# Optimization experiments

Hardware: AMD Instinct MI355X
Metric: run time of the kernel (lower is better)

Reference implementation:

```python
import jax, jax.numpy as jnp
import numpy as np

T = 2048        # q_len (current chunk)
P = 2048        # past KV cache length
HID = 4096      # hidden_size
H = 32          # num_attention_heads
D = HID // H    # head_dim = 128
THETA = 10000.0


def apply_rope(x, pos):
    # x: [H, T, D], pos: [T] int
    half = D // 2
    inv_freq = 1.0 / (THETA ** (jnp.arange(0, half, dtype=jnp.float32) / half))
    ang = pos.astype(jnp.float32)[:, None] * inv_freq[None, :]      # [T, D/2]
    cos = jnp.concatenate([jnp.cos(ang), jnp.cos(ang)], axis=-1)[None]  # [1, T, D]
    sin = jnp.concatenate([jnp.sin(ang), jnp.sin(ang)], axis=-1)[None]
    rot = jnp.concatenate([-x[..., half:], x[..., :half]], axis=-1)
    return x * cos + rot * sin


def setup_inputs() -> dict:
    key = jax.random.key(0)
    ks = jax.random.split(key, 8)
    s = 1.0 / np.sqrt(HID)
    inp = {
        "hidden_states": jax.random.normal(ks[0], (T, HID), dtype=jnp.float32),
        "attention_mask": jnp.triu(jnp.full((T, T), -jnp.inf, dtype=jnp.float32), k=1),
        "Wq": jax.random.normal(ks[1], (HID, HID), dtype=jnp.float32) * s,
        "Wk": jax.random.normal(ks[2], (HID, HID), dtype=jnp.float32) * s,
        "Wv": jax.random.normal(ks[3], (HID, HID), dtype=jnp.float32) * s,
        "Wo": jax.random.normal(ks[4], (HID, HID), dtype=jnp.float32) * s,
        "past_k": jax.random.normal(ks[5], (H, P, D), dtype=jnp.float32),
        "past_v": jax.random.normal(ks[6], (H, P, D), dtype=jnp.float32),
        "position_ids": P + jnp.arange(T, dtype=jnp.int32),
        "past_length": P,
    }
    return inp


def reference(hidden_states, attention_mask, Wq, Wk, Wv, Wo, past_k, past_v,
              position_ids, past_length):
    # QKV projections -> [H, T, D]
    proj = lambda W: (hidden_states @ W).reshape(T, H, D).transpose(1, 0, 2)
    q, k, v = proj(Wq), proj(Wk), proj(Wv)
    q = apply_rope(q, position_ids)
    k = apply_rope(k, position_ids)

    scale = 1.0 / jnp.sqrt(jnp.float32(D))
    # scores against past cache and current chunk (fp32 softmax, as in source)
    past_dots = (jnp.einsum('htd,hsd->hts', q, past_k) * scale).astype(jnp.float32)
    pmask = jnp.where(jnp.arange(P) < past_length, 0.0, -jnp.inf)  # [P]
    past_dots = past_dots + pmask
    cur = ((jnp.einsum('htd,hsd->hts', q, k) * scale) + attention_mask).astype(jnp.float32)

    # online-softmax merge via logsumexp combination
    past_lse = jax.scipy.special.logsumexp(past_dots, axis=-1, keepdims=True)
    cur_lse = jax.scipy.special.logsumexp(cur, axis=-1, keepdims=True)
    tot_lse = jnp.logaddexp(past_lse, cur_lse)
    pw = jnp.exp(past_dots - tot_lse).astype(q.dtype)
    cw = jnp.exp(cur - tot_lse).astype(q.dtype)

    out = jnp.einsum('hts,hsd->htd', pw, past_v) + jnp.einsum('hts,hsd->htd', cw, v)
    out = jnp.where(past_length == 0,
                    jnp.einsum('hts,hsd->htd', jax.nn.softmax(cur, axis=-1).astype(q.dtype), v),
                    out)
    out = out.transpose(1, 0, 2).reshape(T, HID)   # [T, hidden]
    return out @ Wo
```

## Files before the change

kernel.cpp:

```cpp
#include <hip/hip_runtime.h>
#include <cstdint>
#include <cstddef>

#define T_LEN 2048
#define PAST_MAX 2048
#define HID 4096
#define NHEAD 32
#define DHEAD 128

typedef __bf16 bf16_t;
typedef __bf16 bf16x4 __attribute__((ext_vector_type(4)));
typedef __bf16 bf16x8 __attribute__((ext_vector_type(8)));
typedef float  f32x4  __attribute__((ext_vector_type(4)));
typedef float  f32x16 __attribute__((ext_vector_type(16)));
typedef unsigned int u32x4 __attribute__((ext_vector_type(4)));

__device__ __forceinline__ void gload16(const void* g, void* l){
  __builtin_amdgcn_global_load_lds((const __attribute__((address_space(1))) void*)g,
                                   (__attribute__((address_space(3))) void*)l,
                                   16, 0, 0);
}

__device__ __forceinline__ unsigned pack_bf16(float a, float b){
  const unsigned ua = __builtin_bit_cast(unsigned short, (bf16_t)a);
  const unsigned ub = __builtin_bit_cast(unsigned short, (bf16_t)b);
  return ua | (ub << 16);
}

__global__ void cvt2_k(const float* __restrict__ a, bf16_t* __restrict__ ao,
                       const float* __restrict__ b, bf16_t* __restrict__ bo, int n4){
  int i = blockIdx.x * 256 + threadIdx.x;
  if (i < n4){
    const float4 v = ((const float4*)a)[i];
    bf16x4 o = { (bf16_t)v.x, (bf16_t)v.y, (bf16_t)v.z, (bf16_t)v.w };
    ((bf16x4*)ao)[i] = o;
  } else {
    i -= n4;
    const float4 v = ((const float4*)b)[i];
    bf16x4 o = { (bf16_t)v.x, (bf16_t)v.y, (bf16_t)v.z, (bf16_t)v.w };
    ((bf16x4*)bo)[i] = o;
  }
}

__global__ __launch_bounds__(256) void transpose2_k(const float* __restrict__ in,
                                                    bf16_t* __restrict__ out, int R, int C){
  __shared__ float tile[64][65];
  const int r0 = blockIdx.x << 6, c0 = blockIdx.y << 6;
  const size_t bo = (size_t)blockIdx.z * (size_t)R * (size_t)C;
  const int tx = threadIdx.x & 15, ty = threadIdx.x >> 4;
#pragma unroll
  for (int k = 0; k < 4; ++k){
    const float4 v = *(const float4*)(in + bo + (size_t)(r0 + ty + 16*k) * C + c0 + tx*4);
    float* tp = &tile[ty + 16*k][tx*4];
    tp[0] = v.x; tp[1] = v.y; tp[2] = v.z; tp[3] = v.w;
  }
  __syncthreads();
  const int rr0 = (threadIdx.x & 7) * 8;
  const int ccb = threadIdx.x >> 3;
#pragma unroll
  for (int k = 0; k < 2; ++k){
    const int cc = ccb + 32*k;
    bf16x8 o;
#pragma unroll
    for (int j = 0; j < 8; ++j) o[j] = (bf16_t)tile[rr0 + j][cc];
    *(bf16x8*)(out + bo + (size_t)(c0 + cc) * R + r0 + rr0) = o;
  }
}

__global__ __launch_bounds__(256) void transpose3_k(
    const float* __restrict__ s0, const float* __restrict__ s1, const float* __restrict__ s2,
    bf16_t* __restrict__ d0, bf16_t* __restrict__ d1, bf16_t* __restrict__ d2){
  __shared__ float tile[64][65];
  const float* in = (blockIdx.z == 0) ? s0 : (blockIdx.z == 1) ? s1 : s2;
  bf16_t* out = (blockIdx.z == 0) ? d0 : (blockIdx.z == 1) ? d1 : d2;
  const int r0 = blockIdx.x << 6, c0 = blockIdx.y << 6;
  const int tx = threadIdx.x & 15, ty = threadIdx.x >> 4;
#pragma unroll
  for (int k = 0; k < 4; ++k){
    const float4 v = *(const float4*)(in + (size_t)(r0 + ty + 16*k) * HID + c0 + tx*4);
    float* tp = &tile[ty + 16*k][tx*4];
    tp[0] = v.x; tp[1] = v.y; tp[2] = v.z; tp[3] = v.w;
  }
  __syncthreads();
  const int rr0 = (threadIdx.x & 7) * 8;
  const int ccb = threadIdx.x >> 3;
#pragma unroll
  for (int k = 0; k < 2; ++k){
    const int cc = ccb + 32*k;
    bf16x8 o;
#pragma unroll
    for (int j = 0; j < 8; ++j) o[j] = (bf16_t)tile[rr0 + j][cc];
    *(bf16x8*)(out + (size_t)(c0 + cc) * HID + r0 + rr0) = o;
  }
}

__global__ void ropek_k(bf16_t* __restrict__ K, const int* __restrict__ pos){
  const int idx = blockIdx.x * 256 + threadIdx.x;
  const int i = idx & 63;
  const int t = (idx >> 6) & (T_LEN - 1);
  const int h = idx >> 17;
  const size_t base = ((size_t)h * T_LEN + t) * DHEAD;
  const float p = (float)pos[t];
  const float inv = __expf(-(float)i * 0.14391156605212898f);
  const float ang = p * inv;
  float sn, cs;
  sincosf(ang, &sn, &cs);
  const float b0 = (float)K[base + i], b1 = (float)K[base + i + 64];
  K[base + i]      = (bf16_t)(b0 * cs - b1 * sn);
  K[base + i + 64] = (bf16_t)(b1 * cs + b0 * sn);
}

#define QUAD384(PR, BF) \
  __builtin_amdgcn_s_setprio(1); \
  _Pragma("unroll") \
  for (int kk = 0; kk < 2; ++kk){ \
    _Pragma("unroll") \
    for (int mf = 0; mf < 4; ++mf){ \
      _Pragma("unroll") \
      for (int ni = 0; ni < 2; ++ni) \
        acc[mf][(PR)*2 + ni] = __builtin_amdgcn_mfma_f32_16x16x32_bf16( \
            af[mf][kk], BF[ni][kk], acc[mf][(PR)*2 + ni], 0, 0, 0); \
    } \
  } \
  __builtin_amdgcn_s_setprio(0);

__global__ __launch_bounds__(512, 1) void gemmqkv384_k(
    const bf16_t* __restrict__ A,
    const bf16_t* __restrict__ Bc,
    bf16_t* __restrict__ OQ, bf16_t* __restrict__ OK2, bf16_t* __restrict__ OVT)
{
  const int bid = blockIdx.x;
  const int wg  = (bid & 7) * 64 + (bid >> 3);
  const int mt  = wg & 15;
  const int nt  = wg >> 4;
  const int m0  = mt << 7;
  const int n0g = nt * 384;

  const int tid = threadIdx.x;
  const int wv = tid >> 6, lane = tid & 63, lm = lane & 15, g = lane >> 4;
  const int wr = wv >> 2, wc = wv & 3;

  __shared__ __align__(16) char smem[131072];

  const f32x4 fzero = {0.f, 0.f, 0.f, 0.f};
  f32x4 acc[4][6];
#pragma unroll
  for (int i = 0; i < 4; ++i)
#pragma unroll
    for (int j = 0; j < 6; ++j) acc[i][j] = fzero;

  size_t aoff[2], boff[2];
#pragma unroll
  for (int i = 0; i < 2; ++i){
    const int c = i * 512 + tid;
    const int u = c >> 3;
    const int j = ((c & 7) ^ (u & 7)) << 3;
    aoff[i] = (size_t)(m0 + u) * HID + j;
    const int bcol = (u >> 5) * 96 + (u & 31);
    boff[i] = (size_t)(n0g + bcol) * HID + j;
  }
  const int ldst0 = (wv * 64) << 4;
  const int ldst1 = (512 + wv * 64) << 4;

  auto stgA = [&](char* buf, int kt){
    const bf16_t* src = A + (size_t)kt * 64;
    gload16(src + aoff[0], buf + ldst0);
    gload16(src + aoff[1], buf + ldst1);
  };
  auto stgB = [&](char* buf, int kt, int pr){
    const bf16_t* src = Bc + (size_t)kt * 64 + (size_t)pr * (32 * HID);
    char* dst = buf + 16384 + pr * 16384;
    gload16(src + boff[0], dst + ldst0);
    gload16(src + boff[1], dst + ldst1);
  };

  const int koff0 = ((0 + g) ^ (lm & 7)) << 4;
  const int koff1 = ((4 + g) ^ (lm & 7)) << 4;
  const int abase = ((wr << 6) + lm) << 7;
  const int bbase = ((wc << 5) + lm) << 7;

  stgA(smem, 0); stgB(smem, 0, 0); stgB(smem, 0, 1); stgB(smem, 0, 2);
  stgA(smem + 65536, 1); stgB(smem + 65536, 1, 0); stgB(smem + 65536, 1, 1);
  asm volatile("s_waitcnt vmcnt(6)" ::: "memory");
  __builtin_amdgcn_s_barrier();

  bf16x8 af[4][2], bf[2][2];

  for (int kt = 0; kt < 64; ++kt){
    char* buf  = smem + (kt & 1) * 65536;
    char* obuf = smem + ((kt + 1) & 1) * 65536;

#pragma unroll
    for (int mf = 0; mf < 4; ++mf){
      af[mf][0] = *(const bf16x8*)(buf + abase + mf * 2048 + koff0);
      af[mf][1] = *(const bf16x8*)(buf + abase + mf * 2048 + koff1);
    }
#pragma unroll
    for (int ni = 0; ni < 2; ++ni){
      bf[ni][0] = *(const bf16x8*)(buf + 16384 + bbase + ni * 2048 + koff0);
      bf[ni][1] = *(const bf16x8*)(buf + 16384 + bbase + ni * 2048 + koff1);
    }
    if (kt + 1 < 64) stgB(obuf, kt + 1, 2);
    __builtin_amdgcn_sched_barrier(0);
    __builtin_amdgcn_s_barrier();
    asm volatile("s_waitcnt lgkmcnt(0)" ::: "memory");
    __builtin_amdgcn_sched_barrier(0);
    QUAD384(0, bf)
    __builtin_amdgcn_s_barrier();

#pragma unroll
    for (int ni = 0; ni < 2; ++ni){
      bf[ni][0] = *(const bf16x8*)(buf + 32768 + bbase + ni * 2048 + koff0);
      bf[ni][1] = *(const bf16x8*)(buf + 32768 + bbase + ni * 2048 + koff1);
    }
    if (kt + 2 < 64) stgA(buf, kt + 2);
    __builtin_amdgcn_sched_barrier(0);
    __builtin_amdgcn_s_barrier();
    asm volatile("s_waitcnt lgkmcnt(0)" ::: "memory");
    __builtin_amdgcn_sched_barrier(0);
    QUAD384(1, bf)
    __builtin_amdgcn_s_barrier();

#pragma unroll
    for (int ni = 0; ni < 2; ++ni){
      bf[ni][0] = *(const bf16x8*)(buf + 49152 + bbase + ni * 2048 + koff0);
      bf[ni][1] = *(const bf16x8*)(buf + 49152 + bbase + ni * 2048 + koff1);
    }
    if (kt + 2 < 64){ stgB(buf, kt + 2, 0); stgB(buf, kt + 2, 1); }
    __builtin_amdgcn_sched_barrier(0);
    __builtin_amdgcn_s_barrier();
    asm volatile("s_waitcnt lgkmcnt(0)" ::: "memory");
    __builtin_amdgcn_sched_barrier(0);
    QUAD384(2, bf)
    if (kt <= 61) asm volatile("s_waitcnt vmcnt(6)" ::: "memory");
    else          asm volatile("s_waitcnt vmcnt(0)" ::: "memory");
    __builtin_amdgcn_sched_barrier(0);
    __builtin_amdgcn_s_barrier();
  }

#pragma unroll
  for (int pr = 0; pr < 3; ++pr)
#pragma unroll
    for (int ni = 0; ni < 2; ++ni){
      const int colg = n0g + wc * 96 + pr * 32 + ni * 16 + lm;
      const int z  = colg >> 12;
      const int wi = colg & 4095;
      const int hh = wi >> 7, dd = wi & 127;
      const int ai = pr * 2 + ni;
#pragma unroll
      for (int mf = 0; mf < 4; ++mf){
        const int trow0 = m0 + wr * 64 + mf * 16 + g * 4;
        if (z == 2){
          bf16x4 v4 = { (bf16_t)acc[mf][ai][0], (bf16_t)acc[mf][ai][1],
                        (bf16_t)acc[mf][ai][2], (bf16_t)acc[mf][ai][3] };
          *(bf16x4*)(OVT + ((size_t)hh * DHEAD + dd) * T_LEN + trow0) = v4;
        } else {
          bf16_t* ob = z ? OK2 : OQ;
#pragma unroll
          for (int r = 0; r < 4; ++r)
            ob[((size_t)hh * T_LEN + trow0 + r) * DHEAD + dd] = (bf16_t)acc[mf][ai][r];
        }
      }
    }
}

__global__ __launch_bounds__(512, 1) void gemm4p_k(
    const bf16_t* __restrict__ A, const bf16_t* __restrict__ B,
    float* __restrict__ OF, int cpx)
{
  const int bid = blockIdx.x;
  const int wg  = (bid & 7) * cpx + (bid >> 3);
  const int mt  = wg & 7;
  const int nt  = wg >> 3;
  const int m0  = mt << 8;
  const int n0  = nt << 7;

  const int tid = threadIdx.x;
  const int wv = tid >> 6, lane = tid & 63, lm = lane & 15, g = lane >> 4;
  const int wr = wv >> 1, wc = wv & 1;

  __shared__ __align__(16) char smem[98304];

  const f32x4 fzero = {0.f, 0.f, 0.f, 0.f};
  f32x4 acc[4][4];
#pragma unroll
  for (int i = 0; i < 4; ++i)
#pragma unroll
    for (int j = 0; j < 4; ++j) acc[i][j] = fzero;

  int srow[2], schk[2];
#pragma unroll
  for (int i = 0; i < 2; ++i){
    const int c = i * 512 + tid;
    srow[i] = c >> 3;
    schk[i] = (c & 7) ^ (srow[i] & 7);
  }
  const int sdst0 = ((0 * 512 + wv * 64) << 4);
  const int sdst1 = ((1 * 512 + wv * 64) << 4);

  auto stg = [&](int kt, int op){
    if (kt < 64){
      char* dst = smem + (kt & 1) * 49152 + op * 16384;
      const bf16_t* base = (op < 2) ? A + (size_t)(m0 + (op << 7)) * HID
                                    : B + (size_t)n0 * HID;
      base += kt * 64;
      gload16(base + (size_t)srow[0] * HID + schk[0] * 8, dst + sdst0);
      gload16(base + (size_t)srow[1] * HID + schk[1] * 8, dst + sdst1);
    }
  };

  const int koff0 = ((g)     ^ (lm & 7)) << 4;
  const int koff1 = ((4 + g) ^ (lm & 7)) << 4;
  const int abase = ((wr >> 1) << 14) + ((((wr & 1) << 6) + lm) << 7);
  const int bbase = 32768 + ((((wc << 6)) + lm) << 7);

  bf16x8 bfr[4][2];
  auto dsB = [&](int buf){
    const char* p = smem + buf * 49152 + bbase;
#pragma unroll
    for (int ni = 0; ni < 4; ++ni){
      bfr[ni][0] = *(const bf16x8*)(p + ni * 2048 + koff0);
      bfr[ni][1] = *(const bf16x8*)(p + ni * 2048 + koff1);
    }
  };

  stg(0, 2);
  stg(0, 0); stg(0, 1);
  stg(1, 2);
  asm volatile("s_waitcnt vmcnt(2)" ::: "memory");
  __builtin_amdgcn_s_barrier();

  for (int t = 0; t < 32; ++t){
    const int c0 = 2 * t, c1 = 2 * t + 1;
    const bool last = (t == 31);

#pragma unroll
    for (int half = 0; half < 2; ++half){
      const char* bufp = smem + half * 49152;
      bf16x8 afr[2][2];
      dsB(half);
#pragma unroll
      for (int mf = 0; mf < 2; ++mf){
        afr[mf][0] = *(const bf16x8*)(bufp + abase + mf * 2048 + koff0);
        afr[mf][1] = *(const bf16x8*)(bufp + abase + mf * 2048 + koff1);
      }
      if (half == 0){ stg(c1, 0); stg(c1, 1); }
      else          { stg(c0 + 2, 0); stg(c0 + 2, 1); }
      __builtin_amdgcn_s_barrier();
      asm volatile("s_waitcnt lgkmcnt(0)" ::: "memory");
      __builtin_amdgcn_s_setprio(1);
#pragma unroll
      for (int kk = 0; kk < 2; ++kk)
#pragma unroll
        for (int mf = 0; mf < 2; ++mf)
#pragma unroll
          for (int ni = 0; ni < 4; ++ni)
            acc[mf][ni] = __builtin_amdgcn_mfma_f32_16x16x32_bf16(afr[mf][kk], bfr[ni][kk], acc[mf][ni], 0, 0, 0);
      __builtin_amdgcn_s_setprio(0);
      __builtin_amdgcn_s_barrier();

#pragma unroll
      for (int mf = 0; mf < 2; ++mf){
        afr[mf][0] = *(const bf16x8*)(bufp + abase + (mf + 2) * 2048 + koff0);
        afr[mf][1] = *(const bf16x8*)(bufp + abase + (mf + 2) * 2048 + koff1);
      }
      if (half == 0) stg(c0 + 2, 2);
      else           stg(c1 + 2, 2);
      if (last) asm volatile("s_waitcnt vmcnt(0)" ::: "memory");
      else      asm volatile("s_waitcnt vmcnt(2)" ::: "memory");
      __builtin_amdgcn_s_barrier();
      asm volatile("s_waitcnt lgkmcnt(0)" ::: "memory");
      __builtin_amdgcn_s_setprio(1);
#pragma unroll
      for (int kk = 0; kk < 2; ++kk)
#pragma unroll
        for (int mf = 0; mf < 2; ++mf)
#pragma unroll
          for (int ni = 0; ni < 4; ++ni)
            acc[mf + 2][ni] = __builtin_amdgcn_mfma_f32_16x16x32_bf16(afr[mf][kk], bfr[ni][kk], acc[mf + 2][ni], 0, 0, 0);
      __builtin_amdgcn_s_setprio(0);
      __builtin_amdgcn_s_barrier();
    }
  }

#pragma unroll
  for (int ni = 0; ni < 4; ++ni){
    const int col = n0 + wc * 64 + ni * 16 + lm;
#pragma unroll
    for (int mf = 0; mf < 4; ++mf)
#pragma unroll
      for (int r = 0; r < 4; ++r){
        const int trow = m0 + wr * 64 + mf * 16 + g * 4 + r;
        OF[(size_t)trow * HID + col] = acc[mf][ni][r];
      }
  }
}

__global__ __launch_bounds__(256, 2) void attn2_k(
    const bf16_t* __restrict__ Q,
    const bf16_t* __restrict__ Kc,
    const bf16_t* __restrict__ VTc,
    const bf16_t* __restrict__ Kp,
    const bf16_t* __restrict__ VTp,
    bf16_t* __restrict__ Ctx,
    const int* __restrict__ plen_p,
    const int* __restrict__ pos)
{
  const int bid = blockIdx.x;
  const int xcd = bid & 7;
  const int k   = bid >> 3;
  const int ho  = k >> 4;
  const int qraw= k & 15;
  const int h   = (xcd << 2) | ho;
  const int qb  = (ho & 2) ? (15 - qraw) : qraw;

  const int tid = threadIdx.x;
  const int w = tid >> 6, lane = tid & 63, l31 = lane & 31, hi = lane >> 5;
  const int qw0 = qb * 128 + w * 32;
  const int qrow = qw0 + l31;
  const int plen = plen_p[0];
  const int npast = (plen + 63) >> 6;
  const int NT = npast + 2 * qb + 2;

  __shared__ __align__(16) char smem[65536 + 512];
  float* lred = (float*)(smem + 65536);

  const bf16_t* qbase = Q + ((size_t)h * T_LEN + qrow) * DHEAD;
  bf16x8 qf[8];
#pragma unroll
  for (int dc = 0; dc < 8; ++dc)
    qf[dc] = *(const bf16x8*)(qbase + dc * 16 + 8 * hi);
  {
    const float ppos = (float)pos[qrow];
    const float qs = 0.08838834764831845f;
#pragma unroll
    for (int dc = 0; dc < 4; ++dc)
#pragma unroll
      for (int j = 0; j < 8; ++j){
        const int fi = dc * 16 + 8 * hi + j;
        const float invf = __expf(-(float)fi * 0.14391156605212898f);
        float sn, cs;
        sincosf(ppos * invf, &sn, &cs);
        const float a0 = (float)qf[dc][j], a1 = (float)qf[dc + 4][j];
        qf[dc][j]     = (bf16_t)((a0 * cs - a1 * sn) * qs);
        qf[dc + 4][j] = (bf16_t)((a1 * cs + a0 * sn) * qs);
      }
  }
  __builtin_amdgcn_sched_barrier(0);

  const f32x16 fz = {0.f,0.f,0.f,0.f,0.f,0.f,0.f,0.f,0.f,0.f,0.f,0.f,0.f,0.f,0.f,0.f};
  f32x16 o[4] = {fz, fz, fz, fz};
  float m = -1e30f, l = 0.f;

  auto stage = [&](int t, int buf){
    const bf16_t* kb; const bf16_t* vb;
    if (t < npast){
      const int s0 = t * 64;
      kb = Kp  + ((size_t)h * PAST_MAX + s0) * DHEAD;
      vb = VTp + (size_t)h * DHEAD * PAST_MAX + s0;
    } else {
      const int s0 = (t - npast) * 64;
      kb = Kc  + ((size_t)h * T_LEN + s0) * DHEAD;
      vb = VTc + (size_t)h * DHEAD * T_LEN + s0;
    }
    char* kl = smem + buf * 32768;
    char* vl = kl + 16384;
#pragma unroll
    for (int i = 0; i < 4; ++i){
      const int c = i * 256 + w * 64 + lane;
      const int krow = c >> 4, kcol = c & 15;
      gload16(kb + (size_t)krow * DHEAD + ((kcol ^ (krow & 7)) << 3), kl + (i * 256 + w * 64) * 16);
      const int vrow = c >> 3, vcol = c & 7;
      gload16(vb + (size_t)vrow * 2048 + ((vcol ^ (vrow & 7)) << 3), vl + (i * 256 + w * 64) * 16);
    }
  };

  stage(0, 0);
  __builtin_amdgcn_sched_barrier(0);

  for (int t = 0; t < NT; ++t){
    const int cur = t & 1;
    if (t + 1 < NT){
      stage(t + 1, cur ^ 1);
      asm volatile("s_waitcnt vmcnt(8)" ::: "memory");
    } else {
      asm volatile("s_waitcnt vmcnt(0)" ::: "memory");
    }
    __builtin_amdgcn_sched_barrier(0);
    __builtin_amdgcn_s_barrier();
    __builtin_amdgcn_sched_barrier(0);

    const bool isc = (t >= npast);
    const int s0c = (t - npast) * 64;
    const bool active = !isc || (s0c <= qw0 + 31);

    if (active){
      char* kl = smem + cur * 32768;
      char* vl = kl + 16384;

      f32x16 sacc[2] = {fz, fz};
      __builtin_amdgcn_s_setprio(1);
#pragma unroll
      for (int kvh = 0; kvh < 2; ++kvh){
        const int krow = (kvh << 5) + l31;
        const int kbo = krow << 8;
        const int sw = (krow & 7) << 4;
#pragma unroll
        for (int dc = 0; dc < 8; ++dc){
          const bf16x8 kf = *(const bf16x8*)(kl + kbo + ((dc * 32 + 16 * hi) ^ sw));
          sacc[kvh] = __builtin_amdgcn_mfma_f32_32x32x16_bf16(kf, qf[dc], sacc[kvh], 0, 0, 0);
        }
      }
      __builtin_amdgcn_s_setprio(0);

      const bool mcur  = isc && (s0c + 63 > qw0);
      const bool mpast = !isc && ((t + 1) * 64 > plen);
      float pv[2][16];
      float pm = -1e30f;
      if (mcur | mpast){
#pragma unroll
        for (int kvh = 0; kvh < 2; ++kvh)
#pragma unroll
          for (int r = 0; r < 16; ++r){
            float x = sacc[kvh][r];
            const int kvoff = (kvh << 5) + (r & 3) + 8 * (r >> 2) + 4 * hi;
            if (mcur  && (s0c + kvoff >  qrow)) x = -1e30f;
            if (mpast && (t * 64 + kvoff >= plen)) x = -1e30f;
            pv[kvh][r] = x;
            pm = fmaxf(pm, x);
          }
      } else {
#pragma unroll
        for (int kvh = 0; kvh < 2; ++kvh)
#pragma unroll
          for (int r = 0; r < 16; ++r){
            pv[kvh][r] = sacc[kvh][r];
            pm = fmaxf(pm, sacc[kvh][r]);
          }
      }
      pm = fmaxf(pm, __shfl_xor(pm, 32));

      if (!__all(pm - m <= 8.f)){
        const float mn = fmaxf(m, pm);
        const float corr = __expf(m - mn);
        m = mn;
        l *= corr;
        if (hi == 0) lred[(w << 5) + l31] = corr;
        asm volatile("s_waitcnt lgkmcnt(0)" ::: "memory");
#pragma unroll
        for (int r = 0; r < 16; ++r){
          const float cc = lred[(w << 5) + (r & 3) + 8 * (r >> 2) + 4 * hi];
#pragma unroll
          for (int nb = 0; nb < 4; ++nb) o[nb][r] *= cc;
        }
      }

      float sum = 0.f;
#pragma unroll
      for (int kvh = 0; kvh < 2; ++kvh)
#pragma unroll
        for (int r = 0; r < 16; ++r){
          const float pe = __expf(pv[kvh][r] - m);
          pv[kvh][r] = pe;
          sum += pe;
        }
      sum += __shfl_xor(sum, 32);
      l += sum;

      unsigned wds[2][8];
#pragma unroll
      for (int kvh = 0; kvh < 2; ++kvh)
#pragma unroll
        for (int i = 0; i < 8; ++i)
          wds[kvh][i] = pack_bf16(pv[kvh][2 * i], pv[kvh][2 * i + 1]);

      bf16x8 pf[4];
#pragma unroll
      for (int ks = 0; ks < 4; ++ks){
        const int s = ks & 1, kvh = ks >> 1;
        const unsigned a0 = hi ? wds[kvh][4 * s]     : wds[kvh][4 * s + 2];
        const unsigned a1 = hi ? wds[kvh][4 * s + 1] : wds[kvh][4 * s + 3];
        const unsigned z0 = (unsigned)__shfl_xor((int)a0, 32);
        const unsigned z1 = (unsigned)__shfl_xor((int)a1, 32);
        u32x4 fw;
        fw[0] = hi ? z0 : wds[kvh][4 * s];
        fw[1] = hi ? z1 : wds[kvh][4 * s + 1];
        fw[2] = hi ? wds[kvh][4 * s + 2] : z0;
        fw[3] = hi ? wds[kvh][4 * s + 3] : z1;
        pf[ks] = __builtin_bit_cast(bf16x8, fw);
      }

      __builtin_amdgcn_s_setprio(1);
#pragma unroll
      for (int ks = 0; ks < 4; ++ks)
#pragma unroll
        for (int nb = 0; nb < 4; ++nb){
          const int vrow = (nb << 5) + l31;
          const bf16x8 vf = *(const bf16x8*)(vl + (vrow << 7) + ((ks * 32 + 16 * hi) ^ ((vrow & 7) << 4)));
          o[nb] = __builtin_amdgcn_mfma_f32_32x32x16_bf16(pf[ks], vf, o[nb], 0, 0, 0);
        }
      __builtin_amdgcn_s_setprio(0);
    }
    __builtin_amdgcn_sched_barrier(0);
    __builtin_amdgcn_s_barrier();
  }

  if (hi == 0) lred[(w << 5) + l31] = l;
  asm volatile("s_waitcnt lgkmcnt(0)" ::: "memory");
#pragma unroll
  for (int r = 0; r < 16; ++r){
    const int cr = (r & 3) + 8 * (r >> 2) + 4 * hi;
    const float li = 1.f / lred[(w << 5) + cr];
    const int trow = qw0 + cr;
    bf16_t* cb = Ctx + (size_t)trow * HID + h * DHEAD + l31;
#pragma unroll
    for (int nb = 0; nb < 4; ++nb)
      cb[nb << 5] = (bf16_t)(o[nb][r] * li);
  }
}

extern "C" void kernel_launch(void* const* d_in, const int* in_sizes, int n_in,
                              void* d_out, int out_size, void* d_ws, size_t ws_size,
                              hipStream_t stream)
{
  const float* X   = (const float*)d_in[0];
  const float* Wq  = (const float*)d_in[2];
  const float* Wk  = (const float*)d_in[3];
  const float* Wv  = (const float*)d_in[4];
  const float* Wo  = (const float*)d_in[5];
  const float* PKi = (const float*)d_in[6];
  const float* PVi = (const float*)d_in[7];
  const int* POS   = (const int*)d_in[8];
  const int* PLEN  = (const int*)d_in[9];
  float* OUT = (float*)d_out;

  char* ws = (char*)d_ws;
  const size_t SZ_XB  = (size_t)T_LEN * HID * 2;
  const size_t SZ_W   = (size_t)HID * HID * 2;
  const size_t SZ_HTD = (size_t)NHEAD * T_LEN * DHEAD * 2;

  bf16_t* XB  = (bf16_t*)(ws);
  bf16_t* WT0 = (bf16_t*)(ws + SZ_XB);
  bf16_t* WT1 = (bf16_t*)(ws + SZ_XB + SZ_W);
  bf16_t* WT2 = (bf16_t*)(ws + SZ_XB + 2 * SZ_W);
  char* p = ws + SZ_XB + 3 * SZ_W;
  bf16_t* QB   = (bf16_t*)p; p += SZ_HTD;
  bf16_t* KB   = (bf16_t*)p; p += SZ_HTD;
  bf16_t* VTB  = (bf16_t*)p; p += SZ_HTD;
  bf16_t* KPB  = (bf16_t*)p; p += SZ_HTD;
  bf16_t* VPTB = (bf16_t*)p; p += SZ_HTD;
  bf16_t* CTX  = (bf16_t*)p; p += SZ_HTD;
  bf16_t* WOT  = QB;

  dim3 blk256(256);
  dim3 blk512(512);
  cvt2_k<<<16384, blk256, 0, stream>>>(X, XB, PKi, KPB, T_LEN * HID / 4);
  transpose3_k<<<dim3(64,64,3), blk256, 0, stream>>>(Wq, Wk, Wv, WT0, WT1, WT2);
  transpose2_k<<<dim3(32,2,32), blk256, 0, stream>>>(PVi, VPTB, PAST_MAX, DHEAD);

  gemmqkv384_k<<<512, blk512, 0, stream>>>(XB, WT0, QB, KB, VTB);
  ropek_k<<<16384, blk256, 0, stream>>>(KB, POS);
  attn2_k<<<512, blk256, 0, stream>>>(QB, KB, VTB, KPB, VPTB, CTX, PLEN, POS);

  transpose2_k<<<dim3(64,64,1), blk256, 0, stream>>>(Wo, WOT, HID, HID);
  gemm4p_k<<<256, blk512, 0, stream>>>(CTX, WOT, OUT, 32);
}
```

Measured before the change: 535.4 us.

## Retile output projection GEMM to 128x256 and vectorize RoPE-K kernel

The output projection GEMM moves from 256x128 tiles with a two-half A/B split to 128x256 tiles on a 2x4 wave grid. It stages A once per k-step and B in two 32-row pairs, prefetching across a double buffer under explicit vmcnt waits and sched barriers. The RoPE kernel for K now has each thread process 8 contiguous elements with bf16x8 vector loads and stores, using one-eighth as many threads. The intent is to cut LDS traffic and barrier overhead in the GEMM and to cut memory transactions in RoPE, at the cost of tighter pipeline wait accounting.

```diff
diff --git a/kernel.cpp b/kernel.cpp
--- a/kernel.cpp
+++ b/kernel.cpp
@@ -94,20 +94,28 @@
   }
 }
 
-__global__ void ropek_k(bf16_t* __restrict__ K, const int* __restrict__ pos){
+__global__ void ropek8_k(bf16_t* __restrict__ K, const int* __restrict__ pos){
   const int idx = blockIdx.x * 256 + threadIdx.x;
-  const int i = idx & 63;
-  const int t = (idx >> 6) & (T_LEN - 1);
-  const int h = idx >> 17;
+  const int jc = idx & 7;
+  const int t  = (idx >> 3) & (T_LEN - 1);
+  const int h  = idx >> 14;
   const size_t base = ((size_t)h * T_LEN + t) * DHEAD;
   const float p = (float)pos[t];
-  const float inv = __expf(-(float)i * 0.14391156605212898f);
-  const float ang = p * inv;
-  float sn, cs;
-  sincosf(ang, &sn, &cs);
-  const float b0 = (float)K[base + i], b1 = (float)K[base + i + 64];
-  K[base + i]      = (bf16_t)(b0 * cs - b1 * sn);
-  K[base + i + 64] = (bf16_t)(b1 * cs + b0 * sn);
+  bf16x8 lo = *(bf16x8*)(K + base + jc * 8);
+  bf16x8 hi = *(bf16x8*)(K + base + 64 + jc * 8);
+  bf16x8 olo, ohi;
+#pragma unroll
+  for (int j = 0; j < 8; ++j){
+    const int fi = jc * 8 + j;
+    const float invf = __expf(-(float)fi * 0.14391156605212898f);
+    float sn, cs;
+    sincosf(p * invf, &sn, &cs);
+    const float b0 = (float)lo[j], b1 = (float)hi[j];
+    olo[j] = (bf16_t)(b0 * cs - b1 * sn);
+    ohi[j] = (bf16_t)(b1 * cs + b0 * sn);
+  }
+  *(bf16x8*)(K + base + jc * 8) = olo;
+  *(bf16x8*)(K + base + 64 + jc * 8) = ohi;
 }
 
 #define QUAD384(PR, BF) \
@@ -264,20 +272,34 @@
     }
 }
 
-__global__ __launch_bounds__(512, 1) void gemm4p_k(
+#define OPQUAD(PR, BF) \
+  __builtin_amdgcn_s_setprio(1); \
+  _Pragma("unroll") \
+  for (int kk = 0; kk < 2; ++kk){ \
+    _Pragma("unroll") \
+    for (int mf = 0; mf < 4; ++mf){ \
+      _Pragma("unroll") \
+      for (int ni = 0; ni < 2; ++ni) \
+        acc[mf][(PR)*2 + ni] = __builtin_amdgcn_mfma_f32_16x16x32_bf16( \
+            af[mf][kk], BF[ni][kk], acc[mf][(PR)*2 + ni], 0, 0, 0); \
+    } \
+  } \
+  __builtin_amdgcn_s_setprio(0);
+
+__global__ __launch_bounds__(512, 1) void gemmop2p_k(
     const bf16_t* __restrict__ A, const bf16_t* __restrict__ B,
-    float* __restrict__ OF, int cpx)
+    float* __restrict__ OF)
 {
   const int bid = blockIdx.x;
-  const int wg  = (bid & 7) * cpx + (bid >> 3);
-  const int mt  = wg & 7;
-  const int nt  = wg >> 3;
-  const int m0  = mt << 8;
-  const int n0  = nt << 7;
+  const int wg  = (bid & 7) * 32 + (bid >> 3);
+  const int mt  = wg & 15;
+  const int nt  = wg >> 4;
+  const int m0  = mt << 7;
+  const int n0  = nt << 8;
 
   const int tid = threadIdx.x;
   const int wv = tid >> 6, lane = tid & 63, lm = lane & 15, g = lane >> 4;
-  const int wr = wv >> 1, wc = wv & 1;
+  const int wr = wv >> 2, wc = wv & 3;
 
   __shared__ __align__(16) char smem[98304];
 
@@ -288,112 +310,99 @@
 #pragma unroll
     for (int j = 0; j < 4; ++j) acc[i][j] = fzero;
 
-  int srow[2], schk[2];
+  size_t aoff[2], boff[2];
 #pragma unroll
   for (int i = 0; i < 2; ++i){
     const int c = i * 512 + tid;
-    srow[i] = c >> 3;
-    schk[i] = (c & 7) ^ (srow[i] & 7);
-  }
-  const int sdst0 = ((0 * 512 + wv * 64) << 4);
-  const int sdst1 = ((1 * 512 + wv * 64) << 4);
-
-  auto stg = [&](int kt, int op){
-    if (kt < 64){
-      char* dst = smem + (kt & 1) * 49152 + op * 16384;
-      const bf16_t* base = (op < 2) ? A + (size_t)(m0 + (op << 7)) * HID
-                                    : B + (size_t)n0 * HID;
-      base += kt * 64;
-      gload16(base + (size_t)srow[0] * HID + schk[0] * 8, dst + sdst0);
-      gload16(base + (size_t)srow[1] * HID + schk[1] * 8, dst + sdst1);
-    }
+    const int u = c >> 3;
+    const int j = ((c & 7) ^ (u & 7)) << 3;
+    aoff[i] = (size_t)(m0 + u) * HID + j;
+    const int bcol = (u >> 5) * 64 + (u & 31);
+    boff[i] = (size_t)(n0 + bcol) * HID + j;
+  }
+  const int ldst0 = (wv * 64) << 4;
+  const int ldst1 = (512 + wv * 64) << 4;
+
+  auto stgA = [&](char* buf, int kt){
+    const bf16_t* src = A + (size_t)kt * 64;
+    gload16(src + aoff[0], buf + ldst0);
+    gload16(src + aoff[1], buf + ldst1);
   };
-
-  const int koff0 = ((g)     ^ (lm & 7)) << 4;
+  auto stgB = [&](char* buf, int kt, int pr){
+    const bf16_t* src = B + (size_t)kt * 64 + (size_t)pr * (32 * HID);
+    char* dst = buf + 16384 + pr * 16384;
+    gload16(src + boff[0], dst + ldst0);
+    gload16(src + boff[1], dst + ldst1);
+  };
+
+  const int koff0 = ((0 + g) ^ (lm & 7)) << 4;
   const int koff1 = ((4 + g) ^ (lm & 7)) << 4;
-  const int abase = ((wr >> 1) << 14) + ((((wr & 1) << 6) + lm) << 7);
-  const int bbase = 32768 + ((((wc << 6)) + lm) << 7);
-
-  bf16x8 bfr[4][2];
-  auto dsB = [&](int buf){
-    const char* p = smem + buf * 49152 + bbase;
-#pragma unroll
-    for (int ni = 0; ni < 4; ++ni){
-      bfr[ni][0] = *(const bf16x8*)(p + ni * 2048 + koff0);
-      bfr[ni][1] = *(const bf16x8*)(p + ni * 2048 + koff1);
-    }
-  };
-
-  stg(0, 2);
-  stg(0, 0); stg(0, 1);
-  stg(1, 2);
-  asm volatile("s_waitcnt vmcnt(2)" ::: "memory");
+  const int abase = ((wr << 6) + lm) << 7;
+  const int bbase = ((wc << 5) + lm) << 7;
+
+  stgA(smem, 0); stgB(smem, 0, 0); stgB(smem, 0, 1);
+  stgA(smem + 49152, 1); stgB(smem + 49152, 1, 0);
+  asm volatile("s_waitcnt vmcnt(4)" ::: "memory");
   __builtin_amdgcn_s_barrier();
 
-  for (int t = 0; t < 32; ++t){
-    const int c0 = 2 * t, c1 = 2 * t + 1;
-    const bool last = (t == 31);
-
-#pragma unroll
-    for (int half = 0; half < 2; ++half){
-      const char* bufp = smem + half * 49152;
-      bf16x8 afr[2][2];
-      dsB(half);
-#pragma unroll
-      for (int mf = 0; mf < 2; ++mf){
-        afr[mf][0] = *(const bf16x8*)(bufp + abase + mf * 2048 + koff0);
-        afr[mf][1] = *(const bf16x8*)(bufp + abase + mf * 2048 + koff1);
-      }
-      if (half == 0){ stg(c1, 0); stg(c1, 1); }
-      else          { stg(c0 + 2, 0); stg(c0 + 2, 1); }
-      __builtin_amdgcn_s_barrier();
-      asm volatile("s_waitcnt lgkmcnt(0)" ::: "memory");
-      __builtin_amdgcn_s_setprio(1);
-#pragma unroll
-      for (int kk = 0; kk < 2; ++kk)
-#pragma unroll
-        for (int mf = 0; mf < 2; ++mf)
-#pragma unroll
-          for (int ni = 0; ni < 4; ++ni)
-            acc[mf][ni] = __builtin_amdgcn_mfma_f32_16x16x32_bf16(afr[mf][kk], bfr[ni][kk], acc[mf][ni], 0, 0, 0);
-      __builtin_amdgcn_s_setprio(0);
-      __builtin_amdgcn_s_barrier();
-
-#pragma unroll
-      for (int mf = 0; mf < 2; ++mf){
-        afr[mf][0] = *(const bf16x8*)(bufp + abase + (mf + 2) * 2048 + koff0);
-        afr[mf][1] = *(const bf16x8*)(bufp + abase + (mf + 2) * 2048 + koff1);
-      }
-      if (half == 0) stg(c0 + 2, 2);
-      else           stg(c1 + 2, 2);
-      if (last) asm volatile("s_waitcnt vmcnt(0)" ::: "memory");
-      else      asm volatile("s_waitcnt vmcnt(2)" ::: "memory");
-      __builtin_amdgcn_s_barrier();
-      asm volatile("s_waitcnt lgkmcnt(0)" ::: "memory");
-      __builtin_amdgcn_s_setprio(1);
-#pragma unroll
-      for (int kk = 0; kk < 2; ++kk)
-#pragma unroll
-        for (int mf = 0; mf < 2; ++mf)
-#pragma unroll
-          for (int ni = 0; ni < 4; ++ni)
-            acc[mf + 2][ni] = __builtin_amdgcn_mfma_f32_16x16x32_bf16(afr[mf][kk], bfr[ni][kk], acc[mf + 2][ni], 0, 0, 0);
-      __builtin_amdgcn_s_setprio(0);
-      __builtin_amdgcn_s_barrier();
-    }
-  }
-
-#pragma unroll
-  for (int ni = 0; ni < 4; ++ni){
-    const int col = n0 + wc * 64 + ni * 16 + lm;
-#pragma unroll
-    for (int mf = 0; mf < 4; ++mf)
-#pragma unroll
-      for (int r = 0; r < 4; ++r){
-        const int trow = m0 + wr * 64 + mf * 16 + g * 4 + r;
-        OF[(size_t)trow * HID + col] = acc[mf][ni][r];
-      }
-  }
+  bf16x8 af[4][2], bf[2][2];
+
+  for (int kt = 0; kt < 64; ++kt){
+    char* buf  = smem + (kt & 1) * 49152;
+    char* obuf = smem + ((kt + 1) & 1) * 49152;
+
+#pragma unroll
+    for (int mf = 0; mf < 4; ++mf){
+      af[mf][0] = *(const bf16x8*)(buf + abase + mf * 2048 + koff0);
+      af[mf][1] = *(const bf16x8*)(buf + abase + mf * 2048 + koff1);
+    }
+#pragma unroll
+    for (int ni = 0; ni < 2; ++ni){
+      bf[ni][0] = *(const bf16x8*)(buf + 16384 + bbase + ni * 2048 + koff0);
+      bf[ni][1] = *(const bf16x8*)(buf + 16384 + bbase + ni * 2048 + koff1);
+    }
+    if (kt + 1 < 64) stgB(obuf, kt + 1, 1);
+    __builtin_amdgcn_sched_barrier(0);
+    __builtin_amdgcn_s_barrier();
+    asm volatile("s_waitcnt lgkmcnt(0)" ::: "memory");
+    __builtin_amdgcn_sched_barrier(0);
+    OPQUAD(0, bf)
+    if (kt < 62) asm volatile("s_waitcnt vmcnt(6)" ::: "memory");
+    else         asm volatile("s_waitcnt vmcnt(0)" ::: "memory");
+    __builtin_amdgcn_sched_barrier(0);
+    __builtin_amdgcn_s_barrier();
+
+#pragma unroll
+    for (int ni = 0; ni < 2; ++ni){
+      bf[ni][0] = *(const bf16x8*)(buf + 32768 + bbase + ni * 2048 + koff0);
+      bf[ni][1] = *(const bf16x8*)(buf + 32768 + bbase + ni * 2048 + koff1);
+    }
+    if (kt + 2 < 64){ stgA(buf, kt + 2); stgB(buf, kt + 2, 0); }
+    __builtin_amdgcn_sched_barrier(0);
+    __builtin_amdgcn_s_barrier();
+    asm volatile("s_waitcnt lgkmcnt(0)" ::: "memory");
+    __builtin_amdgcn_sched_barrier(0);
+    OPQUAD(1, bf)
+    if (kt < 62) asm volatile("s_waitcnt vmcnt(6)" ::: "memory");
+    else         asm volatile("s_waitcnt vmcnt(0)" ::: "memory");
+    __builtin_amdgcn_sched_barrier(0);
+    __builtin_amdgcn_s_barrier();
+  }
+
+#pragma unroll
+  for (int pr = 0; pr < 2; ++pr)
+#pragma unroll
+    for (int ni = 0; ni < 2; ++ni){
+      const int col = n0 + wc * 64 + pr * 32 + ni * 16 + lm;
+      const int ai = pr * 2 + ni;
+#pragma unroll
+      for (int mf = 0; mf < 4; ++mf)
+#pragma unroll
+        for (int r = 0; r < 4; ++r){
+          const int trow = m0 + wr * 64 + mf * 16 + g * 4 + r;
+          OF[(size_t)trow * HID + col] = acc[mf][ai][r];
+        }
+    }
 }
 
 __global__ __launch_bounds__(256, 2) void attn2_k(
@@ -659,9 +668,9 @@
   transpose2_k<<<dim3(32,2,32), blk256, 0, stream>>>(PVi, VPTB, PAST_MAX, DHEAD);
 
   gemmqkv384_k<<<512, blk512, 0, stream>>>(XB, WT0, QB, KB, VTB);
-  ropek_k<<<16384, blk256, 0, stream>>>(KB, POS);
+  ropek8_k<<<2048, blk256, 0, stream>>>(KB, POS);
   attn2_k<<<512, blk256, 0, stream>>>(QB, KB, VTB, KPB, VPTB, CTX, PLEN, POS);
 
   transpose2_k<<<dim3(64,64,1), blk256, 0, stream>>>(Wo, WOT, HID, HID);
-  gemm4p_k<<<256, blk512, 0, stream>>>(CTX, WOT, OUT, 32);
-}
+  gemmop2p_k<<<256, blk512, 0, stream>>>(CTX, WOT, OUT);
+}
```

Result: no change. 539.2 us (+0.7%).
